# Kernel tuning notes

Hardware: AMD Instinct MI355X
Metric: run time of the kernel (lower is better)

## Reference

```python
import jax, jax.numpy as jnp
from jax import lax
import numpy as np

FEAT_STRIDE = 16
N_PRE_NMS = 6000
N_POST_NMS = 300
NMS_THRESH = 0.7
MIN_SIZE = 16.0
HH, WW = 100, 152  # feature map size
IN_C, MID_C, N_ANCHOR = 512, 512, 9


def _anchor_base(base=16.0, ratios=(0.5, 1.0, 2.0), scales=(8, 16, 32)):
    py, px = base / 2.0, base / 2.0
    ab = np.zeros((len(ratios) * len(scales), 4), np.float32)
    for i, r in enumerate(ratios):
        for j, s in enumerate(scales):
            h = base * s * np.sqrt(r)
            w = base * s * np.sqrt(1.0 / r)
            ab[i * len(scales) + j] = [py - h / 2, px - w / 2, py + h / 2, px + w / 2]
    return ab


def _shifted_anchors(hh, ww, stride=FEAT_STRIDE):
    ab = _anchor_base()
    sy = np.arange(hh, dtype=np.float32) * stride
    sx = np.arange(ww, dtype=np.float32) * stride
    sx, sy = np.meshgrid(sx, sy)
    shift = np.stack((sy.ravel(), sx.ravel(), sy.ravel(), sx.ravel()), axis=1)
    # [K,A,4] -> [K*A,4]: location-major, anchor-minor (matches loc reshape order)
    return (shift[:, None, :] + ab[None, :, :]).reshape(-1, 4).astype(np.float32)


def _conv2d(x, w, b, pad):
    y = lax.conv_general_dilated(x, w, (1, 1), [(pad, pad), (pad, pad)],
                                 dimension_numbers=("NCHW", "OIHW", "NCHW"))
    return y + b[None, :, None, None]


def _loc2bbox(anchor, loc):
    h = anchor[:, 2] - anchor[:, 0]
    w = anchor[:, 3] - anchor[:, 1]
    cy = anchor[:, 0] + 0.5 * h
    cx = anchor[:, 1] + 0.5 * w
    dy, dx, dh, dw = loc[:, 0], loc[:, 1], loc[:, 2], loc[:, 3]
    cy2 = dy * h + cy
    cx2 = dx * w + cx
    h2 = jnp.exp(dh) * h
    w2 = jnp.exp(dw) * w
    return jnp.stack([cy2 - 0.5 * h2, cx2 - 0.5 * w2, cy2 + 0.5 * h2, cx2 + 0.5 * w2], axis=1)


def _nms_keep(boxes, thresh):
    # boxes sorted by score desc; sequential greedy NMS via fori_loop over a
    # precomputed [N,N] IoU matrix.
    N = boxes.shape[0]
    y1, x1, y2, x2 = boxes[:, 0], boxes[:, 1], boxes[:, 2], boxes[:, 3]
    area = (y2 - y1) * (x2 - x1)
    ih = jnp.clip(jnp.minimum(y2[:, None], y2[None, :]) - jnp.maximum(y1[:, None], y1[None, :]), 0.0)
    iw = jnp.clip(jnp.minimum(x2[:, None], x2[None, :]) - jnp.maximum(x1[:, None], x1[None, :]), 0.0)
    inter = ih * iw
    iou = inter / (area[:, None] + area[None, :] - inter + 1e-9)
    idx = jnp.arange(N)

    def body(i, keep):
        sup = keep[i] & (iou[i] > thresh) & (idx > i)
        return keep & ~sup

    return lax.fori_loop(0, N, body, jnp.ones((N,), bool))


def setup_inputs() -> dict:
    key = jax.random.key(0)
    ks = jax.random.split(key, 4)
    return {
        "x": jax.random.normal(ks[0], (1, IN_C, HH, WW), jnp.float32),
        "conv1_w": 0.01 * jax.random.normal(ks[1], (MID_C, IN_C, 3, 3), jnp.float32),
        "conv1_b": jnp.zeros((MID_C,), jnp.float32),
        "score_w": 0.01 * jax.random.normal(ks[2], (N_ANCHOR * 2, MID_C, 1, 1), jnp.float32),
        "score_b": jnp.zeros((N_ANCHOR * 2,), jnp.float32),
        "loc_w": 0.01 * jax.random.normal(ks[3], (N_ANCHOR * 4, MID_C, 1, 1), jnp.float32),
        "loc_b": jnp.zeros((N_ANCHOR * 4,), jnp.float32),
        "img_h": 1600,
        "img_w": 2432,
    }


def reference(x, conv1_w, conv1_b, score_w, score_b, loc_w, loc_b, img_h, img_w):
    n, _, hh, ww = x.shape
    anchors = jnp.asarray(_shifted_anchors(hh, ww))  # [hh*ww*A, 4]

    h = jax.nn.relu(_conv2d(x, conv1_w, conv1_b, 1))
    rpn_loc = _conv2d(h, loc_w, loc_b, 0).transpose(0, 2, 3, 1).reshape(n, -1, 4)
    scores_hw = _conv2d(h, score_w, score_b, 0).transpose(0, 2, 3, 1)  # [n,hh,ww,2A]
    fg = jax.nn.softmax(scores_hw.reshape(n, hh, ww, N_ANCHOR, 2), axis=-1)[..., 1].reshape(n, -1)
    rpn_score = scores_hw.reshape(n, -1, 2)

    # ProposalCreator (single image)
    roi = _loc2bbox(anchors, rpn_loc[0])
    roi = jnp.stack([
        jnp.clip(roi[:, 0], 0.0, img_h), jnp.clip(roi[:, 1], 0.0, img_w),
        jnp.clip(roi[:, 2], 0.0, img_h), jnp.clip(roi[:, 3], 0.0, img_w)], axis=1)
    valid = ((roi[:, 2] - roi[:, 0]) >= MIN_SIZE) & ((roi[:, 3] - roi[:, 1]) >= MIN_SIZE)
    sc = jnp.where(valid, fg[0], -jnp.inf)

    top_sc, order = lax.top_k(sc, N_PRE_NMS)
    roi_s = roi[order]  # sorted by score desc
    keep = _nms_keep(lax.stop_gradient(roi_s), NMS_THRESH) & (top_sc > -jnp.inf)
    sel_sc, sel = lax.top_k(jnp.where(keep, top_sc, -jnp.inf), N_POST_NMS)
    rois = jnp.where((sel_sc > -jnp.inf)[:, None], roi_s[sel], 0.0)  # [N_POST_NMS,4], zero-padded
    return rpn_loc, rpn_score, rois
```

## Files before the change

### kernel.cpp

```cpp
#include <hip/hip_runtime.h>
#include <math.h>
#include <stdint.h>

#define CHH 100
#define CWW 152
#define NPIX 15200
#define NANCH 136800
#define NPRE 6000
#define NPOST 300
#define CANDCAP 8192
#define MROW 96

#define PSTRIDE 154
#define PPVALID 16016
#define PPS 16128
#define XGUARD 256
#define XROWS_TOTAL (PPS + 2*XGUARD)

#define LPAD 32

#define WTH_OFF  0ull
#define WTL_OFF  4718592ull
#define WX_OFF   9437184ull
#define XH_OFF   9547776ull
#define XL_OFF   26587136ull
#define H_OFF    43626496ull
#define ROI_OFF  76656640ull
#define SC_OFF   78845440ull
#define CTL_OFF  79392640ull
#define CAND_OFF 79396736ull
#define SBOX_OFF 79462272ull

typedef _Float16 f16x8 __attribute__((ext_vector_type(8)));
typedef float    f32x4 __attribute__((ext_vector_type(4)));

struct Ctl {
  unsigned hist[256];
  unsigned prefix;
  unsigned countGreater;
  unsigned candCount;
  unsigned done;
};

struct AnchorArg { float v[36]; };

__device__ __forceinline__ unsigned mono_key(float f) {
  unsigned u = __float_as_uint(f);
  return u ^ ((u & 0x80000000u) ? 0xFFFFFFFFu : 0x80000000u);
}

__device__ __forceinline__ void async_copy16(void* lds, const void* g) {
  __builtin_amdgcn_global_load_lds(
      (const __attribute__((address_space(1))) unsigned int*)g,
      (__attribute__((address_space(3))) unsigned int*)lds,
      16, 0, 0);
}

__global__ __launch_bounds__(256) void prep_w_kernel(const float* __restrict__ w1,
                                                     _Float16* __restrict__ wtapH,
                                                     _Float16* __restrict__ wtapL,
                                                     const float* __restrict__ score_w,
                                                     const float* __restrict__ loc_w,
                                                     float* __restrict__ wx,
                                                     Ctl* __restrict__ ctl) {
  __shared__ float wl[4608];
  const int oc = blockIdx.x, tid = threadIdx.x;
  if (oc == 0) {
    ctl->hist[tid] = 0u;
    if (tid == 0) { ctl->prefix = 0u; ctl->countGreater = 0u; ctl->candCount = 0u; ctl->done = 0u; }
  }
  if (tid < 54) wx[oc * 54 + tid] = (tid < 18) ? score_w[tid * 512 + oc] : loc_w[(tid - 18) * 512 + oc];
  for (int li = tid; li < 4608; li += 256) wl[li] = w1[(size_t)oc * 4608 + li];
  __syncthreads();
  for (int t = 0; t < 9; ++t) {
    size_t ob = ((size_t)t * 512 + oc) * 512;
    for (int ic = tid; ic < 512; ic += 256) {
      float v = wl[ic * 9 + t];
      _Float16 hi = (_Float16)v;
      wtapH[ob + ic] = hi;
      wtapL[ob + ic] = (_Float16)(v - (float)hi);
    }
  }
}

__global__ __launch_bounds__(256) void prep_x_kernel(const float* __restrict__ x,
                                                     _Float16* __restrict__ xh,
                                                     _Float16* __restrict__ xl) {
  __shared__ float tile[64][65];
  const int tid = threadIdx.x;
  const int r0 = blockIdx.x * 64;
  for (int ic0 = 0; ic0 < 512; ic0 += 64) {
    #pragma unroll
    for (int it = 0; it < 16; ++it) {
      int li = it * 256 + tid;
      int i = li >> 6, j = li & 63;
      int pp = r0 + j - XGUARD;
      float v = 0.f;
      if (pp >= 0 && pp < PPVALID) {
        int rowp = pp / PSTRIDE, colp = pp - rowp * PSTRIDE;
        if (rowp >= 1 && rowp <= 100 && colp >= 1 && colp <= 152) {
          int p = (rowp - 1) * CWW + (colp - 1);
          v = x[(size_t)(ic0 + i) * NPIX + p];
        }
      }
      tile[i][j] = v;
    }
    __syncthreads();
    int j = tid >> 2, cq = tid & 3;
    size_t ob = (size_t)(r0 + j) * 512 + ic0 + cq * 16;
    f16x8 vh0, vh1, vl0, vl1;
    #pragma unroll
    for (int c = 0; c < 8; ++c) {
      float v = tile[cq * 16 + c][j];
      _Float16 hi = (_Float16)v;
      vh0[c] = hi; vl0[c] = (_Float16)(v - (float)hi);
    }
    #pragma unroll
    for (int c = 0; c < 8; ++c) {
      float v = tile[cq * 16 + 8 + c][j];
      _Float16 hi = (_Float16)v;
      vh1[c] = hi; vl1[c] = (_Float16)(v - (float)hi);
    }
    *(f16x8*)&xh[ob]     = vh0;
    *(f16x8*)&xh[ob + 8] = vh1;
    *(f16x8*)&xl[ob]     = vl0;
    *(f16x8*)&xl[ob + 8] = vl1;
    __syncthreads();
  }
}

__global__ __launch_bounds__(512) void conv1_mfma_kernel(const _Float16* __restrict__ xh,
                                                         const _Float16* __restrict__ xl,
                                                         const _Float16* __restrict__ wtapH,
                                                         const _Float16* __restrict__ wtapL,
                                                         float* __restrict__ h) {
  __shared__ _Float16 Ah[2][256][LPAD], Al[2][256][LPAD], Bh[2][256][LPAD], Bl[2][256][LPAD];
  const int tid = threadIdx.x;
  const int bid = blockIdx.x;
  const int oc0 = (bid & 1) * 256;
  const int KH  = (bid >> 1) & 1;
  const int pp0 = (bid >> 2) * 256;

  const int lane = tid & 63;
  const int n16 = lane & 15, quad = lane >> 4;
  const int wid = tid >> 6;
  const int wm = wid >> 2, wn = wid & 3;
  const int srow = tid >> 2, sq = tid & 3;
  const int wrow = wid << 4;
  const int sqs  = sq ^ ((srow >> 1) & 3);
  const int cswz = (n16 >> 1) & 3;
  const int rdc  = (quad ^ cswz) * 8;

  const size_t thBase = (size_t)srow * 512 + (size_t)sqs * 8;

  f32x4 acc[8][4];
  #pragma unroll
  for (int mi = 0; mi < 8; ++mi)
    #pragma unroll
    for (int ni = 0; ni < 4; ++ni) acc[mi][ni] = (f32x4){0.f, 0.f, 0.f, 0.f};

  auto stageF = [&](int b, int t, int icb, int dsh) {
    const size_t wOff = ((size_t)t * 512 + oc0) * 512 + (size_t)icb;
    const size_t xOff = (size_t)(pp0 + dsh) * 512 + (size_t)icb;
    #pragma unroll
    for (int hf = 0; hf < 2; ++hf) {
      const int lrow = hf * 128 + wrow;
      const size_t tho = thBase + (size_t)(hf * 128) * 512;
      async_copy16(&Ah[b][lrow][0], wtapH + wOff + tho);
      async_copy16(&Al[b][lrow][0], wtapL + wOff + tho);
      async_copy16(&Bh[b][lrow][0], xh + xOff + tho);
      async_copy16(&Bl[b][lrow][0], xl + xOff + tho);
    }
  };

  const int icBase = KH * 256;
  stageF(0, 0, icBase, -PSTRIDE - 1);
  int tS = 1, icbS = icBase, dshS = -PSTRIDE;

  asm volatile("s_waitcnt vmcnt(0)" ::: "memory");
  __builtin_amdgcn_sched_barrier(0);
  __builtin_amdgcn_s_barrier();
  __builtin_amdgcn_sched_barrier(0);

  for (int ks = 0; ks < 72; ++ks) {
    const int cur = ks & 1;
    if (ks + 1 < 72) {
      stageF(cur ^ 1, tS, icbS, dshS);
      if (++tS == 9) { tS = 0; icbS += 32; dshS = -PSTRIDE - 1; }
      else dshS += (tS == 3 || tS == 6) ? (PSTRIDE - 2) : 1;
    }

    __builtin_amdgcn_s_setprio(1);
    f16x8 bf[4], bg[4];
    #pragma unroll
    for (int ni = 0; ni < 4; ++ni) {
      bf[ni] = *(const f16x8*)&Bh[cur][wn * 64 + ni * 16 + n16][rdc];
      bg[ni] = *(const f16x8*)&Bl[cur][wn * 64 + ni * 16 + n16][rdc];
    }
    #pragma unroll
    for (int mi = 0; mi < 8; ++mi) {
      f16x8 af = *(const f16x8*)&Ah[cur][wm * 128 + mi * 16 + n16][rdc];
      f16x8 ag = *(const f16x8*)&Al[cur][wm * 128 + mi * 16 + n16][rdc];
      #pragma unroll
      for (int ni = 0; ni < 4; ++ni) {
        acc[mi][ni] = __builtin_amdgcn_mfma_f32_16x16x32_f16(af, bf[ni], acc[mi][ni], 0, 0, 0);
        acc[mi][ni] = __builtin_amdgcn_mfma_f32_16x16x32_f16(af, bg[ni], acc[mi][ni], 0, 0, 0);
        acc[mi][ni] = __builtin_amdgcn_mfma_f32_16x16x32_f16(ag, bf[ni], acc[mi][ni], 0, 0, 0);
      }
      if (mi == 3) __builtin_amdgcn_sched_barrier(0);
    }
    __builtin_amdgcn_s_setprio(0);

    asm volatile("s_waitcnt lgkmcnt(0) vmcnt(0)" ::: "memory");
    __builtin_amdgcn_sched_barrier(0);
    __builtin_amdgcn_s_barrier();
    __builtin_amdgcn_sched_barrier(0);
  }

  #pragma unroll
  for (int mi = 0; mi < 8; ++mi) {
    int ocb = oc0 + wm * 128 + mi * 16 + quad * 4;
    #pragma unroll
    for (int ni = 0; ni < 4; ++ni) {
      int pp = pp0 + wn * 64 + ni * 16 + n16;
      #pragma unroll
      for (int r = 0; r < 4; ++r)
        atomicAdd(&h[(size_t)(ocb + r) * PPS + pp], acc[mi][ni][r]);
    }
  }
}

__global__ __launch_bounds__(256) void heads_kernel(const float* __restrict__ h,
                                                    const float* __restrict__ conv_b,
                                                    const float* __restrict__ wx,
                                                    const float* __restrict__ score_b,
                                                    const float* __restrict__ loc_b,
                                                    float* __restrict__ rpn_loc,
                                                    float* __restrict__ rpn_score,
                                                    float* __restrict__ roi,
                                                    float* __restrict__ sc,
                                                    AnchorArg ab,
                                                    const int* __restrict__ ihp,
                                                    const int* __restrict__ iwp) {
  __shared__ float hs[64][64];
  __shared__ float red[54][64];
  const int tid = threadIdx.x;
  const int p0 = blockIdx.x * 64;
  const int pxl = tid & 63, icq = tid >> 6;
  int pcol = p0 + pxl;
  bool pok = pcol < NPIX;
  int ppl = 0;
  if (pok) ppl = (pcol / CWW + 1) * PSTRIDE + (pcol % CWW) + 1;

  float acc[54];
  #pragma unroll
  for (int o = 0; o < 54; ++o) acc[o] = 0.f;

  for (int c = 0; c < 8; ++c) {
    int ic0 = c * 64;
    #pragma unroll
    for (int r = 0; r < 16; ++r) {
      int i = r * 4 + icq;
      hs[i][pxl] = pok ? fmaxf(h[(size_t)(ic0 + i) * PPS + ppl] + conv_b[ic0 + i], 0.f) : 0.f;
    }
    __syncthreads();
    #pragma unroll
    for (int k = 0; k < 16; ++k) {
      int icl = icq + k * 4;
      float v = hs[icl][pxl];
      const float* wrow = &wx[(ic0 + icl) * 54];
      #pragma unroll
      for (int o = 0; o < 54; ++o) acc[o] += wrow[o] * v;
    }
    __syncthreads();
  }
  for (int w = 0; w < 4; ++w) {
    if (icq == w) {
      if (w == 0) {
        #pragma unroll
        for (int o = 0; o < 54; ++o) red[o][pxl] = acc[o];
      } else {
        #pragma unroll
        for (int o = 0; o < 54; ++o) red[o][pxl] += acc[o];
      }
    }
    __syncthreads();
  }

  const float fH = (float)(*ihp);
  const float fW = (float)(*iwp);
  for (int it = tid; it < 576; it += 256) {
    #pragma clang fp contract(off)
    int pl = it / 9, a = it - pl * 9;
    int p = p0 + pl;
    if (p >= NPIX) continue;
    float s0 = red[a * 2][pl]     + score_b[a * 2];
    float s1 = red[a * 2 + 1][pl] + score_b[a * 2 + 1];
    float dy = red[18 + a * 4][pl]     + loc_b[a * 4];
    float dx = red[18 + a * 4 + 1][pl] + loc_b[a * 4 + 1];
    float dh = red[18 + a * 4 + 2][pl] + loc_b[a * 4 + 2];
    float dw = red[18 + a * 4 + 3][pl] + loc_b[a * 4 + 3];
    int row = p * 9 + a;
    *(float2*)&rpn_score[row * 2] = make_float2(s0, s1);
    *(float4*)&rpn_loc[(size_t)row * 4] = make_float4(dy, dx, dh, dw);
    int ypix = p / CWW, xpix = p - ypix * CWW;
    float sy = (float)(ypix * 16), sx = (float)(xpix * 16);
    float a0 = sy + ab.v[a * 4 + 0], a1 = sx + ab.v[a * 4 + 1];
    float a2 = sy + ab.v[a * 4 + 2], a3 = sx + ab.v[a * 4 + 3];
    float ha = a2 - a0, wa = a3 - a1;
    float cy = a0 + 0.5f * ha, cx = a1 + 0.5f * wa;
    float cy2 = dy * ha + cy, cx2 = dx * wa + cx;
    float h2 = expf(dh) * ha, w2 = expf(dw) * wa;
    float y1 = cy2 - 0.5f * h2, x1 = cx2 - 0.5f * w2;
    float y2 = cy2 + 0.5f * h2, x2 = cx2 + 0.5f * w2;
    y1 = fminf(fmaxf(y1, 0.f), fH); x1 = fminf(fmaxf(x1, 0.f), fW);
    y2 = fminf(fmaxf(y2, 0.f), fH); x2 = fminf(fmaxf(x2, 0.f), fW);
    *(float4*)&roi[(size_t)row * 4] = make_float4(y1, x1, y2, x2);
    bool valid = (y2 - y1 >= 16.f) && (x2 - x1 >= 16.f);
    float m  = fmaxf(s0, s1);
    float e0 = expf(s0 - m), e1 = expf(s1 - m);
    float fg = e1 / (e0 + e1);
    sc[row] = valid ? fg : -__builtin_inff();
  }
}

#define HGRID 120
__global__ __launch_bounds__(256) void hist_scan_kernel(const float* __restrict__ sc,
                                                        Ctl* __restrict__ ctl, int pass) {
  __shared__ unsigned hloc[256];
  __shared__ unsigned ticket_s;
  int tid = threadIdx.x;
  hloc[tid] = 0u;
  __syncthreads();
  unsigned prefix = ctl->prefix;
  for (int i = blockIdx.x * 256 + tid; i < NANCH; i += HGRID * 256) {
    unsigned m = mono_key(sc[i]);
    bool pred = (pass == 0) || ((m >> (32 - 8 * pass)) == prefix);
    if (pred) atomicAdd(&hloc[(m >> (24 - 8 * pass)) & 255u], 1u);
  }
  __syncthreads();
  if (hloc[tid]) atomicAdd(&ctl->hist[tid], hloc[tid]);
  __threadfence();
  __syncthreads();
  if (tid == 0) ticket_s = atomicAdd(&ctl->done, 1u);
  __syncthreads();
  if (ticket_s != HGRID - 1) return;
  unsigned v = atomicExch(&ctl->hist[tid], 0u);
  hloc[tid] = v;
  __syncthreads();
  for (int d = 1; d < 256; d <<= 1) {
    unsigned t2 = hloc[tid] + ((tid + d < 256) ? hloc[tid + d] : 0u);
    __syncthreads();
    hloc[tid] = t2;
    __syncthreads();
  }
  unsigned G = ctl->countGreater;
  unsigned inclT = hloc[tid];
  unsigned inclN = (tid < 255) ? hloc[tid + 1] : 0u;
  if (G + inclT >= (unsigned)NPRE && G + inclN < (unsigned)NPRE) {
    ctl->prefix = (prefix << 8) | (unsigned)tid;
    ctl->countGreater = G + inclN;
  }
  if (tid == 0) atomicExch(&ctl->done, 0u);
}

__global__ __launch_bounds__(256) void compact_kernel(const float* __restrict__ sc,
                                                      Ctl* __restrict__ ctl,
                                                      unsigned long long* __restrict__ cand) {
  int i = blockIdx.x * 256 + threadIdx.x;
  unsigned prefix = ctl->prefix;
  bool pred = false; unsigned m = 0;
  if (i < NANCH) { m = mono_key(sc[i]); pred = ((m >> 8) >= prefix); }
  unsigned long long mask = __ballot(pred);
  if (mask) {
    int lane = threadIdx.x & 63;
    int leader = __ffsll((long long)mask) - 1;
    unsigned base = 0;
    if (lane == leader) base = atomicAdd(&ctl->candCount, (unsigned)__popcll(mask));
    base = __shfl(base, leader);
    if (pred) {
      unsigned slot = base + (unsigned)__popcll(mask & ((1ull << lane) - 1ull));
      if (slot < CANDCAP)
        cand[slot] = (((unsigned long long)(~m)) << 32) | (unsigned)i;
    }
  }
}

__global__ __launch_bounds__(256) void rank_kernel(const unsigned long long* __restrict__ cand,
                                                   const Ctl* __restrict__ ctl,
                                                   const float* __restrict__ roi,
                                                   float4* __restrict__ sbox) {
  __shared__ unsigned long long kb[2048];
  __shared__ unsigned pc[64][5];
  const int tid = threadIdx.x;
  const int c = tid & 63, q = tid >> 6;
  const int slot = blockIdx.x * 64 + c;
  unsigned nv = ctl->candCount; if (nv > CANDCAP) nv = CANDCAP;
  unsigned long long K = (slot < (int)nv) ? cand[slot] : ~0ull;
  unsigned cnt = 0;
  for (unsigned c0 = 0; c0 < nv; c0 += 2048) {
    for (int i = tid; i < 2048; i += 256) {
      unsigned g = c0 + (unsigned)i;
      kb[i] = (g < nv) ? cand[g] : ~0ull;
    }
    __syncthreads();
    int lim = (int)(nv - c0); if (lim > 2048) lim = 2048;
    int i0 = q * 512, ie = i0 + 512; if (ie > lim) ie = lim;
    for (int i = i0; i < ie; ++i) cnt += (kb[i] < K) ? 1u : 0u;
    __syncthreads();
  }
  pc[c][q] = cnt;
  __syncthreads();
  if (q == 0) {
    unsigned rank = pc[c][0] + pc[c][1] + pc[c][2] + pc[c][3];
    if (slot < (int)nv && rank < NPRE) {
      unsigned idx = (unsigned)(K & 0xFFFFFFFFull);
      sbox[rank] = *(const float4*)&roi[(size_t)idx * 4];
    }
  } else if (q == 1) {
    int nvR = (nv < (unsigned)NPRE) ? (int)nv : NPRE;
    if (slot >= nvR && slot < NPRE) sbox[slot] = make_float4(0.f, 0.f, 0.f, 0.f);
  }
}

__device__ __forceinline__ bool iou_gt(float4 A, float4 B) {
  float areaA = (A.z - A.x) * (A.w - A.y);
  float areaB = (B.z - B.x) * (B.w - B.y);
  float ih = fmaxf(fminf(A.z, B.z) - fmaxf(A.x, B.x), 0.f);
  float iw = fmaxf(fminf(A.w, B.w) - fmaxf(A.y, B.y), 0.f);
  float inter = ih * iw;
  return inter / (areaA + areaB - inter + 1e-9f) > 0.7f;
}

__global__ __launch_bounds__(64) void mask_kernel(const float4* __restrict__ sbox,
                                                  unsigned long long* __restrict__ M) {
  const int ci = blockIdx.x, cj = blockIdx.y;
  if (cj < ci) return;
  __shared__ float4 cb[64];
  const int tid = threadIdx.x;
  const int i = ci * 64 + tid;
  const int jbase = cj * 64;
  const float4 bi = (i < NPRE) ? sbox[i] : make_float4(0.f, 0.f, 0.f, 0.f);
  cb[tid] = (jbase + tid < NPRE) ? sbox[jbase + tid] : make_float4(0.f, 0.f, 0.f, 0.f);
  __syncthreads();
  if (i >= NPRE) return;
  unsigned long long bits = 0ull;
  #pragma unroll 8
  for (int jj = 0; jj < 64; ++jj) {
    int jg = jbase + jj;
    float4 bj = cb[jj];
    if (jg > i && jg < NPRE && iou_gt(bi, bj)) bits |= (1ull << jj);
  }
  M[(size_t)i * MROW + cj] = bits;
}

__global__ __launch_bounds__(64) void resolve_kernel(const unsigned long long* __restrict__ M,
                                                     const Ctl* __restrict__ ctl,
                                                     const float4* __restrict__ sbox,
                                                     float* __restrict__ rois_out) {
  __shared__ unsigned long long remLDS[94];
  __shared__ int keepList[NPOST];
  __shared__ int keepCount;
  const int l = threadIdx.x;
  unsigned cnt = ctl->candCount; if (cnt > (unsigned)NPRE) cnt = NPRE;
  const int nvalid = (int)cnt;

  auto initw = [&](int w) -> unsigned long long {
    int lo = w * 64;
    if (lo + 64 <= nvalid) return 0ull;
    if (lo >= nvalid) return ~0ull;
    return (~0ull) << (nvalid - lo);
  };
  unsigned long long rem0 = initw(l);
  unsigned long long rem1 = (l < 30) ? initw(64 + l) : ~0ull;

  int keepTotal = 0;
  int cstop = 94;
  unsigned long long dw = M[(size_t)l * MROW + 0];

  for (int c = 0; c < 94; ++c) {
    unsigned long long dwN = 0ull;
    if (c + 1 < 94) dwN = M[(size_t)((c + 1) * 64 + l) * MROW + (c + 1)];

    unsigned long long remRep = (c < 64) ? __shfl(rem0, c) : __shfl(rem1, c - 64);

    #pragma unroll
    for (int kk = 0; kk < 64; kk += 16) {
      unsigned long long wv[16];
      #pragma unroll
      for (int t = 0; t < 16; ++t) wv[t] = __shfl(dw, kk + t);
      #pragma unroll
      for (int t = 0; t < 16; ++t) {
        if (!((remRep >> (kk + t)) & 1ull)) remRep |= wv[t];
      }
    }

    if (l == 0) remLDS[c] = remRep;
    if (c < 64) { if (l == c) rem0 = remRep; }
    else        { if (l == c - 64) rem1 = remRep; }
    keepTotal += (int)__popcll(~remRep);

    unsigned long long km = ~remRep;
    const size_t base = (size_t)c * 64;
    while (km) {
      int k0 = __ffsll((long long)km) - 1; km &= km - 1;
      int k1 = k0, k2 = k0, k3 = k0;
      if (km) { k1 = __ffsll((long long)km) - 1; km &= km - 1; }
      if (km) { k2 = __ffsll((long long)km) - 1; km &= km - 1; }
      if (km) { k3 = __ffsll((long long)km) - 1; km &= km - 1; }
      const unsigned long long* p0 = M + (base + k0) * MROW;
      const unsigned long long* p1 = M + (base + k1) * MROW;
      const unsigned long long* p2 = M + (base + k2) * MROW;
      const unsigned long long* p3 = M + (base + k3) * MROW;
      unsigned long long a0 = p0[l], a1 = p1[l], a2 = p2[l], a3 = p3[l];
      rem0 |= a0 | a1 | a2 | a3;
      if (l < 30) {
        unsigned long long b0 = p0[64 + l], b1 = p1[64 + l], b2 = p2[64 + l], b3 = p3[64 + l];
        rem1 |= b0 | b1 | b2 | b3;
      }
    }

    dw = dwN;
    if (keepTotal >= NPOST) { cstop = c + 1; break; }
  }

  __syncthreads();
  if (l == 0) {
    int ck = 0;
    for (int w = 0; w < cstop && ck < NPOST; ++w) {
      unsigned long long kw = ~remLDS[w];
      while (kw && ck < NPOST) {
        int r = __ffsll((long long)kw) - 1; kw &= kw - 1;
        keepList[ck++] = w * 64 + r;
      }
    }
    keepCount = ck;
  }
  __syncthreads();
  for (int s = l; s < NPOST; s += 64) {
    float4 b = make_float4(0.f, 0.f, 0.f, 0.f);
    if (s < keepCount) b = sbox[keepList[s]];
    *(float4*)&rois_out[(size_t)s * 4] = b;
  }
}

extern "C" void kernel_launch(void* const* d_in, const int* in_sizes, int n_in,
                              void* d_out, int out_size, void* d_ws, size_t ws_size,
                              hipStream_t stream) {
  const float* x  = (const float*)d_in[0];
  const float* w1 = (const float*)d_in[1];
  const float* b1 = (const float*)d_in[2];
  const float* sw = (const float*)d_in[3];
  const float* sb = (const float*)d_in[4];
  const float* lw = (const float*)d_in[5];
  const float* lb = (const float*)d_in[6];
  const int* ihp  = (const int*)d_in[7];
  const int* iwp  = (const int*)d_in[8];
  float* out = (float*)d_out;

  char* ws = (char*)d_ws;
  _Float16* wtapH = (_Float16*)(ws + WTH_OFF);
  _Float16* wtapL = (_Float16*)(ws + WTL_OFF);
  float* wx   = (float*)(ws + WX_OFF);
  _Float16* xh_alloc = (_Float16*)(ws + XH_OFF);
  _Float16* xl_alloc = (_Float16*)(ws + XL_OFF);
  _Float16* xh = xh_alloc + (size_t)XGUARD * 512;
  _Float16* xl = xl_alloc + (size_t)XGUARD * 512;
  float* h    = (float*)(ws + H_OFF);
  float* roi  = (float*)(ws + ROI_OFF);
  float* sc   = (float*)(ws + SC_OFF);
  Ctl*   ctl  = (Ctl*)(ws + CTL_OFF);
  unsigned long long* cand = (unsigned long long*)(ws + CAND_OFF);
  float4* sbox = (float4*)(ws + SBOX_OFF);
  unsigned long long* Mmask = (unsigned long long*)(ws + H_OFF);

  AnchorArg ab;
  {
    const double ratios[3] = {0.5, 1.0, 2.0};
    const double scales[3] = {8.0, 16.0, 32.0};
    for (int i = 0; i < 3; ++i)
      for (int j = 0; j < 3; ++j) {
        double hh = 16.0 * scales[j] * sqrt(ratios[i]);
        double wwd = 16.0 * scales[j] * sqrt(1.0 / ratios[i]);
        int a = i * 3 + j;
        ab.v[a * 4 + 0] = (float)(8.0 - hh / 2.0);
        ab.v[a * 4 + 1] = (float)(8.0 - wwd / 2.0);
        ab.v[a * 4 + 2] = (float)(8.0 + hh / 2.0);
        ab.v[a * 4 + 3] = (float)(8.0 + wwd / 2.0);
      }
  }

  float* rpn_loc   = out;
  float* rpn_score = out + 547200;
  float* rois      = out + 820800;

  prep_w_kernel<<<512, 256, 0, stream>>>(w1, wtapH, wtapL, sw, lw, wx, ctl);
  prep_x_kernel<<<XROWS_TOTAL / 64, 256, 0, stream>>>(x, xh_alloc, xl_alloc);
  hipMemsetAsync(h, 0, (size_t)512 * PPS * sizeof(float), stream);
  conv1_mfma_kernel<<<252, 512, 0, stream>>>(xh, xl, wtapH, wtapL, h);
  heads_kernel<<<238, 256, 0, stream>>>(h, b1, wx, sb, lb, rpn_loc, rpn_score, roi, sc, ab, ihp, iwp);
  for (int p = 0; p < 3; ++p)
    hist_scan_kernel<<<HGRID, 256, 0, stream>>>(sc, ctl, p);
  compact_kernel<<<535, 256, 0, stream>>>(sc, ctl, cand);
  rank_kernel<<<CANDCAP / 64, 256, 0, stream>>>(cand, ctl, roi, sbox);
  mask_kernel<<<dim3(94, 94), 64, 0, stream>>>(sbox, Mmask);
  resolve_kernel<<<1, 64, 0, stream>>>(Mmask, ctl, sbox, rois);
}
```

Before: 679.2 us.

## Interleave LDS fragment loads with MFMA phases and request two blocks per CU

The conv1 MFMA main loop is split into four phases of two M-tiles each. Each phase preloads its A fragments from LDS, then runs its MFMAs under workgroup barriers in a ping-pong schedule, and the global wait for the next stage moves to the last phase. Launch bounds now ask for two 512-thread blocks per CU, which caps registers per thread and may cause spills. In the heads kernel, readfirstlane makes the channel index wave-uniform so the weight row loads can become scalar loads.

```diff
diff --git a/kernel.cpp b/kernel.cpp
--- a/kernel.cpp
+++ b/kernel.cpp
@@ -129,11 +129,11 @@
   }
 }
 
-__global__ __launch_bounds__(512) void conv1_mfma_kernel(const _Float16* __restrict__ xh,
-                                                         const _Float16* __restrict__ xl,
-                                                         const _Float16* __restrict__ wtapH,
-                                                         const _Float16* __restrict__ wtapL,
-                                                         float* __restrict__ h) {
+__global__ __launch_bounds__(512, 2) void conv1_mfma_kernel(const _Float16* __restrict__ xh,
+                                                            const _Float16* __restrict__ xl,
+                                                            const _Float16* __restrict__ wtapH,
+                                                            const _Float16* __restrict__ wtapL,
+                                                            float* __restrict__ h) {
   __shared__ _Float16 Ah[2][256][LPAD], Al[2][256][LPAD], Bh[2][256][LPAD], Bl[2][256][LPAD];
   const int tid = threadIdx.x;
   const int bid = blockIdx.x;
@@ -184,37 +184,72 @@
 
   for (int ks = 0; ks < 72; ++ks) {
     const int cur = ks & 1;
+
+    f16x8 bf[4], bg[4];
+    #pragma unroll
+    for (int ni = 0; ni < 4; ++ni) {
+      bf[ni] = *(const f16x8*)&Bh[cur][wn * 64 + ni * 16 + n16][rdc];
+      bg[ni] = *(const f16x8*)&Bl[cur][wn * 64 + ni * 16 + n16][rdc];
+    }
+    f16x8 af0 = *(const f16x8*)&Ah[cur][wm * 128 + 0 * 16 + n16][rdc];
+    f16x8 ag0 = *(const f16x8*)&Al[cur][wm * 128 + 0 * 16 + n16][rdc];
+    f16x8 af1 = *(const f16x8*)&Ah[cur][wm * 128 + 1 * 16 + n16][rdc];
+    f16x8 ag1 = *(const f16x8*)&Al[cur][wm * 128 + 1 * 16 + n16][rdc];
     if (ks + 1 < 72) {
       stageF(cur ^ 1, tS, icbS, dshS);
       if (++tS == 9) { tS = 0; icbS += 32; dshS = -PSTRIDE - 1; }
       else dshS += (tS == 3 || tS == 6) ? (PSTRIDE - 2) : 1;
     }
-
+    __builtin_amdgcn_s_barrier();
+    asm volatile("s_waitcnt lgkmcnt(0)" ::: "memory");
+    __builtin_amdgcn_sched_barrier(0);
     __builtin_amdgcn_s_setprio(1);
-    f16x8 bf[4], bg[4];
     #pragma unroll
     for (int ni = 0; ni < 4; ++ni) {
-      bf[ni] = *(const f16x8*)&Bh[cur][wn * 64 + ni * 16 + n16][rdc];
-      bg[ni] = *(const f16x8*)&Bl[cur][wn * 64 + ni * 16 + n16][rdc];
-    }
-    #pragma unroll
-    for (int mi = 0; mi < 8; ++mi) {
-      f16x8 af = *(const f16x8*)&Ah[cur][wm * 128 + mi * 16 + n16][rdc];
-      f16x8 ag = *(const f16x8*)&Al[cur][wm * 128 + mi * 16 + n16][rdc];
+      acc[0][ni] = __builtin_amdgcn_mfma_f32_16x16x32_f16(af0, bf[ni], acc[0][ni], 0, 0, 0);
+      acc[0][ni] = __builtin_amdgcn_mfma_f32_16x16x32_f16(af0, bg[ni], acc[0][ni], 0, 0, 0);
+      acc[0][ni] = __builtin_amdgcn_mfma_f32_16x16x32_f16(ag0, bf[ni], acc[0][ni], 0, 0, 0);
+    }
+    #pragma unroll
+    for (int ni = 0; ni < 4; ++ni) {
+      acc[1][ni] = __builtin_amdgcn_mfma_f32_16x16x32_f16(af1, bf[ni], acc[1][ni], 0, 0, 0);
+      acc[1][ni] = __builtin_amdgcn_mfma_f32_16x16x32_f16(af1, bg[ni], acc[1][ni], 0, 0, 0);
+      acc[1][ni] = __builtin_amdgcn_mfma_f32_16x16x32_f16(ag1, bf[ni], acc[1][ni], 0, 0, 0);
+    }
+    __builtin_amdgcn_s_setprio(0);
+    __builtin_amdgcn_sched_barrier(0);
+    __builtin_amdgcn_s_barrier();
+
+    #pragma unroll
+    for (int p = 1; p < 4; ++p) {
+      const int m0 = 2 * p;
+      f16x8 afA = *(const f16x8*)&Ah[cur][wm * 128 + m0 * 16 + n16][rdc];
+      f16x8 agA = *(const f16x8*)&Al[cur][wm * 128 + m0 * 16 + n16][rdc];
+      f16x8 afB = *(const f16x8*)&Ah[cur][wm * 128 + (m0 + 1) * 16 + n16][rdc];
+      f16x8 agB = *(const f16x8*)&Al[cur][wm * 128 + (m0 + 1) * 16 + n16][rdc];
+      if (p == 3) {
+        asm volatile("s_waitcnt vmcnt(0)" ::: "memory");
+      }
+      __builtin_amdgcn_s_barrier();
+      asm volatile("s_waitcnt lgkmcnt(0)" ::: "memory");
+      __builtin_amdgcn_sched_barrier(0);
+      __builtin_amdgcn_s_setprio(1);
       #pragma unroll
       for (int ni = 0; ni < 4; ++ni) {
-        acc[mi][ni] = __builtin_amdgcn_mfma_f32_16x16x32_f16(af, bf[ni], acc[mi][ni], 0, 0, 0);
-        acc[mi][ni] = __builtin_amdgcn_mfma_f32_16x16x32_f16(af, bg[ni], acc[mi][ni], 0, 0, 0);
-        acc[mi][ni] = __builtin_amdgcn_mfma_f32_16x16x32_f16(ag, bf[ni], acc[mi][ni], 0, 0, 0);
-      }
-      if (mi == 3) __builtin_amdgcn_sched_barrier(0);
-    }
-    __builtin_amdgcn_s_setprio(0);
-
-    asm volatile("s_waitcnt lgkmcnt(0) vmcnt(0)" ::: "memory");
-    __builtin_amdgcn_sched_barrier(0);
-    __builtin_amdgcn_s_barrier();
-    __builtin_amdgcn_sched_barrier(0);
+        acc[m0][ni] = __builtin_amdgcn_mfma_f32_16x16x32_f16(afA, bf[ni], acc[m0][ni], 0, 0, 0);
+        acc[m0][ni] = __builtin_amdgcn_mfma_f32_16x16x32_f16(afA, bg[ni], acc[m0][ni], 0, 0, 0);
+        acc[m0][ni] = __builtin_amdgcn_mfma_f32_16x16x32_f16(agA, bf[ni], acc[m0][ni], 0, 0, 0);
+      }
+      #pragma unroll
+      for (int ni = 0; ni < 4; ++ni) {
+        acc[m0 + 1][ni] = __builtin_amdgcn_mfma_f32_16x16x32_f16(afB, bf[ni], acc[m0 + 1][ni], 0, 0, 0);
+        acc[m0 + 1][ni] = __builtin_amdgcn_mfma_f32_16x16x32_f16(afB, bg[ni], acc[m0 + 1][ni], 0, 0, 0);
+        acc[m0 + 1][ni] = __builtin_amdgcn_mfma_f32_16x16x32_f16(agB, bf[ni], acc[m0 + 1][ni], 0, 0, 0);
+      }
+      __builtin_amdgcn_s_setprio(0);
+      __builtin_amdgcn_sched_barrier(0);
+      __builtin_amdgcn_s_barrier();
+    }
   }
 
   #pragma unroll
@@ -247,6 +282,7 @@
   const int tid = threadIdx.x;
   const int p0 = blockIdx.x * 64;
   const int pxl = tid & 63, icq = tid >> 6;
+  const int icu = __builtin_amdgcn_readfirstlane(icq);
   int pcol = p0 + pxl;
   bool pok = pcol < NPIX;
   int ppl = 0;
@@ -266,7 +302,7 @@
     __syncthreads();
     #pragma unroll
     for (int k = 0; k < 16; ++k) {
-      int icl = icq + k * 4;
+      int icl = icu + k * 4;
       float v = hs[icl][pxl];
       const float* wrow = &wx[(ic0 + icl) * 54];
       #pragma unroll
```

Result: no change. 670.4 us (-1.3%).
